# Kernel tuning notes

Measured on AMD Instinct MI355X. Metric: run time of the kernel, lower is better.

Reference implementation:

```python
import jax, jax.numpy as jnp
import numpy as np

B, S, D, H = 32, 8192, 256, 256


def setup_inputs() -> dict:
    key = jax.random.key(0)
    ks = jax.random.split(key, 8)
    # start token: module uses np.random.seed(42); np.random.random([B,1,D])
    rng = np.random.RandomState(42)
    start_token = jnp.asarray(rng.random_sample((B, 1, D)).astype(np.float32))
    s = 0.05  # weight init scale
    return {
        "encoder_output": jax.random.normal(ks[0], (B, S, D), jnp.float32),
        "h0": jax.random.normal(ks[1], (B, H), jnp.float32),
        "c0": jax.random.normal(ks[2], (B, H), jnp.float32),
        "start_token": start_token,
        # Keras LSTM params: kernel [D,4H], recurrent_kernel [H,4H], bias [4H]; gate order i,f,c,o
        "W_k": jax.random.normal(ks[3], (D, 4 * H), jnp.float32) * s,
        "W_r": jax.random.normal(ks[4], (H, 4 * H), jnp.float32) * s,
        "b_lstm": jnp.zeros((4 * H,), jnp.float32),
        # encoder_weight Dense(H), decode_weight Dense(H), v Dense(1)
        "W_e": jax.random.normal(ks[5], (D, H), jnp.float32) * s,
        "b_e": jnp.zeros((H,), jnp.float32),
        "W_d": jax.random.normal(ks[6], (H, H), jnp.float32) * s,
        "b_d": jnp.zeros((H,), jnp.float32),
        "v_w": jax.random.normal(ks[7], (H, 1), jnp.float32) * s,
        "v_b": jnp.zeros((1,), jnp.float32),
    }


def reference(encoder_output, h0, c0, start_token, W_k, W_r, b_lstm,
              W_e, b_e, W_d, b_d, v_w, v_b):
    # --- one Keras-LSTM step on the start token (seq_len = 1) ---
    x = start_token[:, 0, :]                      # [B, D]
    z = x @ W_k + h0 @ W_r + b_lstm               # [B, 4H]
    i, f, g, o = jnp.split(z, 4, axis=-1)         # Keras gate order i,f,c,o
    c = jax.nn.sigmoid(f) * c0 + jax.nn.sigmoid(i) * jnp.tanh(g)
    h = jax.nn.sigmoid(o) * jnp.tanh(c)           # [B, H] decoder output
    # --- Bahdanau additive attention (vectorized form of the double loop) ---
    dec_proj = h @ W_d + b_d                      # [B, H]
    enc_proj = encoder_output @ W_e + b_e         # [B, S, H]
    # tanh(enc_proj + dec_proj) projected to scalar by v
    scores = jnp.tanh(enc_proj + dec_proj[:, None, :]) @ v_w  # [B, S, 1]
    scores = scores[..., 0] + v_b                 # [B, S]
    return jax.nn.softmax(scores, axis=-1)
```

## Files before the change

### kernel.cpp

```cpp
#include <hip/hip_runtime.h>
#include <hip/hip_bf16.h>
#include <stdint.h>

#define B 32
#define S 8192
#define D 256
#define H 256
#define LDA 264

typedef __attribute__((ext_vector_type(8))) short bf16x8;
typedef __attribute__((ext_vector_type(4))) float f32x4;

__device__ inline unsigned short f2bf(float f) {
  unsigned u = __float_as_uint(f);
  unsigned r = (u + 0x7FFFu + ((u >> 16) & 1u)) >> 16;
  return (unsigned short)r;
}

__device__ inline float fast_tanh(float x) {
  float e = __expf(2.0f * x);
  return 1.0f - 2.0f * __builtin_amdgcn_rcpf(1.0f + e);
}

__global__ __launch_bounds__(1024) void prep_kernel(
    const float* __restrict__ h0, const float* __restrict__ c0,
    const float* __restrict__ start_token, const float* __restrict__ W_k,
    const float* __restrict__ W_r, const float* __restrict__ b_lstm,
    const float* __restrict__ W_e, const float* __restrict__ W_d,
    const float* __restrict__ b_d,
    unsigned short* __restrict__ Wfrag, float* __restrict__ dec) {
  int blk = blockIdx.x;
  int tid = threadIdx.x;

  __shared__ float xs[D], hs[H], zs[4 * H], hv[H], dpp[4][H];

  if (blk < 64) {
    int gid = blk * 1024 + tid;
    int j = gid & 7;
    int lane = (gid >> 3) & 63;
    int kt = (gid >> 9) & 7;
    int nt = gid >> 12;
    int n = nt * 16 + (lane & 15);
    int k = kt * 32 + (lane >> 4) * 8 + j;
    Wfrag[gid] = f2bf(W_e[k * H + n]);
  } else {
    int b = blk - 64;
    if (tid < D) xs[tid] = start_token[b * D + tid];
    else if (tid < 2 * D) hs[tid - D] = h0[b * H + (tid - D)];
    __syncthreads();
    {
      int jj = tid;
      float a0 = 0.f, a1 = 0.f, a2 = 0.f, a3 = 0.f;
      #pragma unroll 8
      for (int d = 0; d < D; d += 4) {
        a0 += xs[d + 0] * W_k[(d + 0) * 1024 + jj];
        a1 += xs[d + 1] * W_k[(d + 1) * 1024 + jj];
        a2 += xs[d + 2] * W_k[(d + 2) * 1024 + jj];
        a3 += xs[d + 3] * W_k[(d + 3) * 1024 + jj];
      }
      #pragma unroll 8
      for (int h = 0; h < H; h += 4) {
        a0 += hs[h + 0] * W_r[(h + 0) * 1024 + jj];
        a1 += hs[h + 1] * W_r[(h + 1) * 1024 + jj];
        a2 += hs[h + 2] * W_r[(h + 2) * 1024 + jj];
        a3 += hs[h + 3] * W_r[(h + 3) * 1024 + jj];
      }
      zs[jj] = b_lstm[jj] + ((a0 + a1) + (a2 + a3));
    }
    __syncthreads();
    if (tid < H) {
      float zi = zs[tid], zf = zs[H + tid], zg = zs[2 * H + tid], zo = zs[3 * H + tid];
      float si = 1.0f / (1.0f + expf(-zi));
      float sf = 1.0f / (1.0f + expf(-zf));
      float so = 1.0f / (1.0f + expf(-zo));
      float c = sf * c0[b * H + tid] + si * tanhf(zg);
      hv[tid] = so * tanhf(c);
    }
    __syncthreads();
    {
      int hcol = tid & (H - 1);
      int q = tid >> 8;
      float a = 0.f;
      #pragma unroll 8
      for (int k = q * 64; k < q * 64 + 64; ++k) a += hv[k] * W_d[k * H + hcol];
      dpp[q][hcol] = a;
    }
    __syncthreads();
    if (tid < H)
      dec[b * H + tid] = dpp[0][tid] + dpp[1][tid] + dpp[2][tid] + dpp[3][tid] + b_d[tid];
  }
}

__global__ __launch_bounds__(256, 2) void attn_kernel(
    const float* __restrict__ enc, const unsigned short* __restrict__ Wfrag,
    const float* __restrict__ dec, const float* __restrict__ b_e,
    const float* __restrict__ v_w, float* __restrict__ scores) {
  __shared__ unsigned short Ash[64 * LDA];
  __shared__ float bias_sh[H], vw_sh[H], part_sh[4][64];

  int tid = threadIdx.x;
  int b = blockIdx.x >> 7;
  int st = blockIdx.x & 127;
  long row0 = (long)b * S + st * 64;
  const float* Abase = enc + row0 * (long)D;

  bias_sh[tid] = b_e[tid] + dec[b * H + tid];
  vw_sh[tid] = v_w[tid];

  {
    int r = tid >> 2;
    int c4 = (tid & 3) * 4;
    const float* src = Abase + r * D;
    unsigned short* dst = Ash + r * LDA;
    #pragma unroll
    for (int jj = 0; jj < 16; ++jj) {
      int c = c4 + jj * 16;
      float4 v = *(const float4*)(src + c);
      ushort4 o;
      o.x = f2bf(v.x); o.y = f2bf(v.y); o.z = f2bf(v.z); o.w = f2bf(v.w);
      *(ushort4*)(dst + c) = o;
    }
  }
  __syncthreads();

  int wave = tid >> 6, lane = tid & 63;
  int ml = lane & 15, kg = lane >> 4;

  f32x4 acc[4][4];
  #pragma unroll
  for (int i = 0; i < 4; ++i)
    #pragma unroll
    for (int q = 0; q < 4; ++q) acc[i][q] = (f32x4){0.f, 0.f, 0.f, 0.f};

  #pragma unroll
  for (int kt = 0; kt < 8; ++kt) {
    bf16x8 wfr[4], afr[4];
    #pragma unroll
    for (int q = 0; q < 4; ++q) {
      int nt = wave * 4 + q;
      const unsigned short* p = Wfrag + (((nt * 8 + kt) * 64 + lane) << 3);
      wfr[q] = *(const bf16x8*)p;
    }
    #pragma unroll
    for (int i = 0; i < 4; ++i) {
      const unsigned short* p = Ash + (i * 16 + ml) * LDA + kt * 32 + kg * 8;
      afr[i] = *(const bf16x8*)p;
    }
    #pragma unroll
    for (int i = 0; i < 4; ++i)
      #pragma unroll
      for (int q = 0; q < 4; ++q)
        acc[i][q] = __builtin_amdgcn_mfma_f32_16x16x32_bf16(afr[i], wfr[q], acc[i][q], 0, 0, 0);
  }

  float part[16];
  #pragma unroll
  for (int v = 0; v < 16; ++v) part[v] = 0.f;
  #pragma unroll
  for (int q = 0; q < 4; ++q) {
    int n = wave * 64 + q * 16 + ml;
    float bs = bias_sh[n], vw = vw_sh[n];
    #pragma unroll
    for (int i = 0; i < 4; ++i)
      #pragma unroll
      for (int r = 0; r < 4; ++r) {
        float t = fast_tanh(acc[i][q][r] + bs);
        part[i * 4 + r] += t * vw;
      }
  }
  #pragma unroll
  for (int m = 1; m < 16; m <<= 1)
    #pragma unroll
    for (int v = 0; v < 16; ++v) part[v] += __shfl_xor(part[v], m, 64);
  if (ml == 0) {
    #pragma unroll
    for (int i = 0; i < 4; ++i)
      #pragma unroll
      for (int r = 0; r < 4; ++r)
        part_sh[wave][i * 16 + kg * 4 + r] = part[i * 4 + r];
  }
  __syncthreads();
  if (tid < 64) {
    float s = part_sh[0][tid] + part_sh[1][tid] + part_sh[2][tid] + part_sh[3][tid];
    scores[row0 + tid] = s;
  }
}

__global__ __launch_bounds__(1024) void softmax_kernel(
    const float* __restrict__ scores, float* __restrict__ out) {
  int b = blockIdx.x;
  int tid = threadIdx.x;
  __shared__ float red[16];
  const float* src = scores + (long)b * S;
  float v[8];
  float lmax = -1e30f;
  #pragma unroll
  for (int j = 0; j < 8; ++j) {
    v[j] = src[tid + j * 1024];
    lmax = fmaxf(lmax, v[j]);
  }
  #pragma unroll
  for (int m = 1; m < 64; m <<= 1) lmax = fmaxf(lmax, __shfl_xor(lmax, m, 64));
  if ((tid & 63) == 0) red[tid >> 6] = lmax;
  __syncthreads();
  float M = red[0];
  #pragma unroll
  for (int i = 1; i < 16; ++i) M = fmaxf(M, red[i]);
  __syncthreads();
  float ls = 0.f;
  #pragma unroll
  for (int j = 0; j < 8; ++j) {
    v[j] = __expf(v[j] - M);
    ls += v[j];
  }
  #pragma unroll
  for (int m = 1; m < 64; m <<= 1) ls += __shfl_xor(ls, m, 64);
  if ((tid & 63) == 0) red[tid >> 6] = ls;
  __syncthreads();
  float total = 0.f;
  #pragma unroll
  for (int i = 0; i < 16; ++i) total += red[i];
  float inv = __builtin_amdgcn_rcpf(total);
  #pragma unroll
  for (int j = 0; j < 8; ++j) out[(long)b * S + tid + j * 1024] = v[j] * inv;
}

extern "C" void kernel_launch(void* const* d_in, const int* in_sizes, int n_in,
                              void* d_out, int out_size, void* d_ws, size_t ws_size,
                              hipStream_t stream) {
  const float* enc         = (const float*)d_in[0];
  const float* h0          = (const float*)d_in[1];
  const float* c0          = (const float*)d_in[2];
  const float* start_token = (const float*)d_in[3];
  const float* W_k         = (const float*)d_in[4];
  const float* W_r         = (const float*)d_in[5];
  const float* b_lstm      = (const float*)d_in[6];
  const float* W_e         = (const float*)d_in[7];
  const float* b_e         = (const float*)d_in[8];
  const float* W_d         = (const float*)d_in[9];
  const float* b_d         = (const float*)d_in[10];
  const float* v_w         = (const float*)d_in[11];
  float* out = (float*)d_out;

  char* wsb = (char*)d_ws;
  float* scores         = (float*)wsb;
  unsigned short* Wfrag = (unsigned short*)(wsb + (size_t)B * S * 4);
  float* dec            = (float*)(wsb + (size_t)B * S * 4 + (size_t)D * H * 2);

  prep_kernel<<<96, 1024, 0, stream>>>(h0, c0, start_token, W_k, W_r, b_lstm,
                                       W_e, W_d, b_d, Wfrag, dec);
  attn_kernel<<<B * (S / 64), 256, 0, stream>>>(enc, Wfrag, dec, b_e, v_w, scores);
  softmax_kernel<<<B, 1024, 0, stream>>>(scores, out);
}
```

Before: 450.5 us.

## Load encoder rows directly into MFMA fragments, dropping LDS staging

The attention kernel no longer stages the 64x256 encoder tile through shared memory as bf16. Each lane now loads its A fragment straight from global memory and packs it to bf16 in registers. The wave layout changes from 4 waves each owning 64 columns to a 2x2 split of 32 rows by 128 columns, and the bias and v weights are held in registers. This removes the LDS round trip and one barrier, at the cost of less coalesced global loads (32-byte strided pieces per lane) and more registers for 16 accumulators and 8 weight fragments.

```diff
diff --git a/kernel.cpp b/kernel.cpp
--- a/kernel.cpp
+++ b/kernel.cpp
@@ -6,7 +6,6 @@
 #define S 8192
 #define D 256
 #define H 256
-#define LDA 264
 
 typedef __attribute__((ext_vector_type(8))) short bf16x8;
 typedef __attribute__((ext_vector_type(4))) float f32x4;
@@ -15,6 +14,22 @@
   unsigned u = __float_as_uint(f);
   unsigned r = (u + 0x7FFFu + ((u >> 16) & 1u)) >> 16;
   return (unsigned short)r;
+}
+
+__device__ inline unsigned pk2bf(float a, float b) {
+  __hip_bfloat162 h = __float22bfloat162_rn(make_float2(a, b));
+  unsigned u;
+  __builtin_memcpy(&u, &h, 4);
+  return u;
+}
+
+__device__ inline bf16x8 pack8(float4 a, float4 b) {
+  union { unsigned u[4]; bf16x8 v; } c;
+  c.u[0] = pk2bf(a.x, a.y);
+  c.u[1] = pk2bf(a.z, a.w);
+  c.u[2] = pk2bf(b.x, b.y);
+  c.u[3] = pk2bf(b.z, b.w);
+  return c.v;
 }
 
 __device__ inline float fast_tanh(float x) {
@@ -95,95 +110,80 @@
     const float* __restrict__ enc, const unsigned short* __restrict__ Wfrag,
     const float* __restrict__ dec, const float* __restrict__ b_e,
     const float* __restrict__ v_w, float* __restrict__ scores) {
-  __shared__ unsigned short Ash[64 * LDA];
-  __shared__ float bias_sh[H], vw_sh[H], part_sh[4][64];
+  __shared__ float part_sh[2][64];
 
   int tid = threadIdx.x;
   int b = blockIdx.x >> 7;
   int st = blockIdx.x & 127;
   long row0 = (long)b * S + st * 64;
-  const float* Abase = enc + row0 * (long)D;
-
-  bias_sh[tid] = b_e[tid] + dec[b * H + tid];
-  vw_sh[tid] = v_w[tid];
-
-  {
-    int r = tid >> 2;
-    int c4 = (tid & 3) * 4;
-    const float* src = Abase + r * D;
-    unsigned short* dst = Ash + r * LDA;
-    #pragma unroll
-    for (int jj = 0; jj < 16; ++jj) {
-      int c = c4 + jj * 16;
-      float4 v = *(const float4*)(src + c);
-      ushort4 o;
-      o.x = f2bf(v.x); o.y = f2bf(v.y); o.z = f2bf(v.z); o.w = f2bf(v.w);
-      *(ushort4*)(dst + c) = o;
-    }
-  }
-  __syncthreads();
 
   int wave = tid >> 6, lane = tid & 63;
   int ml = lane & 15, kg = lane >> 4;
-
-  f32x4 acc[4][4];
-  #pragma unroll
-  for (int i = 0; i < 4; ++i)
-    #pragma unroll
-    for (int q = 0; q < 4; ++q) acc[i][q] = (f32x4){0.f, 0.f, 0.f, 0.f};
+  int wr = wave >> 1, wc = wave & 1;
+
+  const float* arow0 = enc + (row0 + wr * 32 + ml) * (long)D + kg * 8;
+  const float* arow1 = arow0 + 16 * D;
+
+  float bs[8], vw8[8];
+  #pragma unroll
+  for (int q = 0; q < 8; ++q) {
+    int n = wc * 128 + q * 16 + ml;
+    bs[q] = b_e[n] + dec[b * H + n];
+    vw8[q] = v_w[n];
+  }
+
+  f32x4 acc[2][8];
+  #pragma unroll
+  for (int i = 0; i < 2; ++i)
+    #pragma unroll
+    for (int q = 0; q < 8; ++q) acc[i][q] = (f32x4){0.f, 0.f, 0.f, 0.f};
 
   #pragma unroll
   for (int kt = 0; kt < 8; ++kt) {
-    bf16x8 wfr[4], afr[4];
-    #pragma unroll
-    for (int q = 0; q < 4; ++q) {
-      int nt = wave * 4 + q;
-      const unsigned short* p = Wfrag + (((nt * 8 + kt) * 64 + lane) << 3);
+    bf16x8 wfr[8];
+    #pragma unroll
+    for (int q = 0; q < 8; ++q) {
+      const unsigned short* p = Wfrag + ((size_t)(((wc * 8 + q) * 8 + kt) * 64 + lane) << 3);
       wfr[q] = *(const bf16x8*)p;
     }
-    #pragma unroll
-    for (int i = 0; i < 4; ++i) {
-      const unsigned short* p = Ash + (i * 16 + ml) * LDA + kt * 32 + kg * 8;
-      afr[i] = *(const bf16x8*)p;
-    }
-    #pragma unroll
-    for (int i = 0; i < 4; ++i)
-      #pragma unroll
-      for (int q = 0; q < 4; ++q)
-        acc[i][q] = __builtin_amdgcn_mfma_f32_16x16x32_bf16(afr[i], wfr[q], acc[i][q], 0, 0, 0);
-  }
-
-  float part[16];
-  #pragma unroll
-  for (int v = 0; v < 16; ++v) part[v] = 0.f;
-  #pragma unroll
-  for (int q = 0; q < 4; ++q) {
-    int n = wave * 64 + q * 16 + ml;
-    float bs = bias_sh[n], vw = vw_sh[n];
-    #pragma unroll
-    for (int i = 0; i < 4; ++i)
-      #pragma unroll
-      for (int r = 0; r < 4; ++r) {
-        float t = fast_tanh(acc[i][q][r] + bs);
-        part[i * 4 + r] += t * vw;
-      }
-  }
-  #pragma unroll
-  for (int m = 1; m < 16; m <<= 1)
-    #pragma unroll
-    for (int v = 0; v < 16; ++v) part[v] += __shfl_xor(part[v], m, 64);
-  if (ml == 0) {
-    #pragma unroll
-    for (int i = 0; i < 4; ++i)
+    float4 a0lo = *(const float4*)(arow0 + kt * 32);
+    float4 a0hi = *(const float4*)(arow0 + kt * 32 + 4);
+    float4 a1lo = *(const float4*)(arow1 + kt * 32);
+    float4 a1hi = *(const float4*)(arow1 + kt * 32 + 4);
+    bf16x8 afr0 = pack8(a0lo, a0hi);
+    bf16x8 afr1 = pack8(a1lo, a1hi);
+    #pragma unroll
+    for (int q = 0; q < 8; ++q) {
+      acc[0][q] = __builtin_amdgcn_mfma_f32_16x16x32_bf16(afr0, wfr[q], acc[0][q], 0, 0, 0);
+      acc[1][q] = __builtin_amdgcn_mfma_f32_16x16x32_bf16(afr1, wfr[q], acc[1][q], 0, 0, 0);
+    }
+  }
+
+  float part[8];
+  #pragma unroll
+  for (int v = 0; v < 8; ++v) part[v] = 0.f;
+  #pragma unroll
+  for (int q = 0; q < 8; ++q) {
+    #pragma unroll
+    for (int i = 0; i < 2; ++i)
       #pragma unroll
       for (int r = 0; r < 4; ++r)
-        part_sh[wave][i * 16 + kg * 4 + r] = part[i * 4 + r];
-  }
-  __syncthreads();
-  if (tid < 64) {
-    float s = part_sh[0][tid] + part_sh[1][tid] + part_sh[2][tid] + part_sh[3][tid];
-    scores[row0 + tid] = s;
-  }
+        part[i * 4 + r] += fast_tanh(acc[i][q][r] + bs[q]) * vw8[q];
+  }
+  #pragma unroll
+  for (int m = 1; m < 16; m <<= 1)
+    #pragma unroll
+    for (int v = 0; v < 8; ++v) part[v] += __shfl_xor(part[v], m, 64);
+  if (ml == 0) {
+    #pragma unroll
+    for (int i = 0; i < 2; ++i)
+      #pragma unroll
+      for (int r = 0; r < 4; ++r)
+        part_sh[wc][wr * 32 + i * 16 + kg * 4 + r] = part[i * 4 + r];
+  }
+  __syncthreads();
+  if (tid < 64)
+    scores[row0 + tid] = part_sh[0][tid] + part_sh[1][tid];
 }
 
 __global__ __launch_bounds__(1024) void softmax_kernel(
```

New measurement: 500.4 us. +11.1%, slower.
